# Performance work log

Measured on AMD Instinct MI355X. Metric: run time of the kernel, lower is better.

Reference implementation:

```python
import jax, jax.numpy as jnp
import numpy as np

B, LD, LQ = 32, 512, 32
E, NF = 300, 4
D = E + NF            # doc_input_size = 304
M = 16                # fofe_max_length == max_len
ALPHA = 0.9
VOCAB = 50000
H = 256
SAMPLE_NUM = 256
POS_N = 128           # int(sample_num * (1 - neg_ratio))
NEG_N = SAMPLE_NUM - POS_N
R = min(M, LD - 2)    # candidate negative lengths = 16
PPL = NEG_N // R + 1  # negatives drawn per length = 9


def setup_inputs() -> dict:
    key = jax.random.key(0)
    ks = jax.random.split(key, 16)
    emb = jax.random.normal(ks[0], (VOCAB, E), jnp.float32) * 0.1
    emb = emb.at[0].set(0.0)  # padding_idx=0
    doc = jax.random.randint(ks[1], (B, LD), 1, VOCAB)
    doc_f = jax.random.normal(ks[2], (B, LD, NF), jnp.float32) * 0.1
    query = jax.random.randint(ks[3], (B, LQ), 1, VOCAB)
    target_s = jax.random.randint(ks[4], (B,), 1, LD - M - 2)
    span = jax.random.randint(ks[5], (B,), 0, M)  # ans_span = target_e - target_s < fofe_max_length
    target_e = target_s + span
    rand_length = jax.random.permutation(ks[6], R)  # torch.randperm(min(max_len, L-2))
    # rand_position[i] ~ randint(1, LD - rand_length[i] - 1)
    u = jax.random.uniform(ks[7], (R, PPL))
    size = (LD - rand_length - 2).astype(jnp.float32)[:, None]
    rand_position = 1 + jnp.floor(u * size).astype(jnp.int32)
    rand_idx = jax.random.randint(ks[8], (NEG_N,), 0, B)  # faithful to original (dim-0 size used as bound)
    perm_idx = jax.random.permutation(ks[9], SAMPLE_NUM)

    def w(k, o, i):
        return jax.random.normal(k, (o, i), jnp.float32) * (1.0 / np.sqrt(i))

    CIN = 3 * D + E  # 1212
    W1 = w(ks[10], 4 * H, CIN)
    W2 = w(ks[11], 4 * H, 4 * H)
    W3 = w(ks[12], 4 * H, 4 * H)
    W4 = w(ks[13], 2 * H, 4 * H)
    W5 = w(ks[14], 1, 2 * H)
    doc_mask = jnp.zeros((B, LD), bool)
    query_mask = jnp.zeros((B, LQ), bool)
    return dict(doc=doc, doc_f=doc_f, query=query, target_s=target_s, target_e=target_e,
                doc_mask=doc_mask, query_mask=query_mask, emb=emb,
                W1=W1, W2=W2, W3=W3, W4=W4, W5=W5,
                rand_length=rand_length, rand_position=rand_position,
                rand_idx=rand_idx, perm_idx=perm_idx)


def _fofe_codes(x):
    """x: [B, D, LD] -> forward/inverse FOFE codes [B, D, M, LD].
    fwd[b,c,l,t] = sum_{k=0}^{l} alpha^k x[b,c,t-k]; inv mirrors to the right."""
    fwd_terms = jnp.stack(
        [(ALPHA ** k) * jnp.pad(x, ((0, 0), (0, 0), (k, 0)))[..., :LD] for k in range(M)], axis=2)
    inv_terms = jnp.stack(
        [(ALPHA ** k) * jnp.pad(x, ((0, 0), (0, 0), (0, k)))[..., k:] for k in range(M)], axis=2)
    return jnp.cumsum(fwd_terms, axis=2), jnp.cumsum(inv_terms, axis=2)


def _cnn(x, W1, W2, W3, W4, W5):
    h = jax.nn.relu(jnp.einsum('oi,bis->bos', W1, x))
    h = jax.nn.relu(jnp.einsum('oi,bis->bos', W2, h))
    h = jax.nn.relu(jnp.einsum('oi,bis->bos', W3, h))
    h = jax.nn.relu(jnp.einsum('oi,bis->bos', W4, h))
    return jax.nn.sigmoid(jnp.einsum('oi,bis->bos', W5, h))


def reference(doc, doc_f, query, target_s, target_e, doc_mask, query_mask, emb,
              W1, W2, W3, W4, W5, rand_length, rand_position, rand_idx, perm_idx):
    # input_embedding (dropout_emb = 0, pos/ner disabled)
    doc_input = jnp.concatenate([emb[doc], doc_f], axis=-1)  # [B, LD, D]
    x = jnp.swapaxes(doc_input, 1, 2)                         # [B, D, LD]
    fwd, inv = _fofe_codes(x)                                 # [B, D, M, LD] each

    # --- positive samples: gold span + left/right full contexts ---
    b = jnp.arange(B)
    span = target_e - target_s
    ans = fwd[b, :, span, target_e]                               # [B, D]
    l_ctx = fwd[b, :, M - 1, jnp.maximum(target_s - 1, 0)]        # [B, D]
    r_ctx = inv[b, :, M - 1, jnp.minimum(target_e + 1, LD - 1)]   # [B, D]
    pos = jnp.concatenate([l_ctx, ans, r_ctx], axis=-1)          # [B, 3D]
    pos = jnp.broadcast_to(pos[:, :, None], (B, 3 * D, POS_N))

    # --- negative samples: random spans of each length in rand_length ---
    rl = rand_length[:, None]                                     # [R, 1]
    neg_ans = fwd[:, :, rl, rand_position].reshape(B, D, R * PPL)
    neg_l = fwd[:, :, M - 1, rand_position - 1].reshape(B, D, R * PPL)
    neg_r = inv[:, :, M - 1, rand_position + rl + 1].reshape(B, D, R * PPL)
    rand_cat = jnp.concatenate([neg_l, neg_ans, neg_r], axis=1)   # [B, 3D, R*PPL]
    neg = rand_cat[:, :, rand_idx]                                # [B, 3D, NEG_N]

    # --- shuffle pos+neg, build query FOFE, run cnn, mse (sum) loss ---
    ctx_ans = jnp.concatenate([pos, neg], axis=-1)[:, :, perm_idx]
    target = jnp.concatenate(
        [jnp.ones((B, 1, POS_N), jnp.float32), jnp.zeros((B, 1, NEG_N), jnp.float32)],
        axis=-1)[:, :, perm_idx]
    qw = ALPHA ** jnp.arange(LQ - 1, -1, -1, dtype=jnp.float32)   # fofe_linear weights
    qf = jnp.einsum('t,bte->be', qw, emb[query])                  # [B, E]
    qb = jnp.broadcast_to(qf[:, :, None], (B, E, SAMPLE_NUM))
    dq_input = jnp.concatenate([ctx_ans, qb], axis=1)             # [B, 3D+E, S]
    score = _cnn(dq_input, W1, W2, W3, W4, W5)                    # [B, 1, S]
    loss = jnp.sum((score - target) ** 2)                         # mse_loss(size_average=False)
    return loss
```

## Files before the change

kernel.cpp:

```cpp
#include <hip/hip_runtime.h>
#include <hip/hip_bf16.h>

#define B_    32
#define LD_   512
#define LQ_   32
#define E_    300
#define NF_   4
#define D_    304
#define M_    16
#define ALPHA_ 0.9f
#define CIN_  1212
#define KP1_  1216
#define NCOL_ 1056
#define NPAD_ 1088
#define PPL_  9
#define NEG_N_ 128

typedef short short8 __attribute__((ext_vector_type(8)));
typedef float f32x4 __attribute__((ext_vector_type(4)));

__device__ __forceinline__ unsigned short f2bf(float f) {
    unsigned int x = __float_as_uint(f);
    unsigned int r = (x + 0x7FFFu + ((x >> 16) & 1u)) >> 16;
    return (unsigned short)r;
}
__device__ __forceinline__ float bf2f(unsigned short u) {
    return __uint_as_float(((unsigned int)u) << 16);
}

__global__ __launch_bounds__(256) void build_features(
    const int* __restrict__ doc, const float* __restrict__ doc_f,
    const int* __restrict__ query, const int* __restrict__ target_s,
    const int* __restrict__ target_e, const float* __restrict__ emb,
    const int* __restrict__ rand_length, const int* __restrict__ rand_position,
    unsigned short* __restrict__ Ft)
{
    int bcol = blockIdx.x;
    int b = bcol / 33;
    int col = bcol % 33;
    __shared__ int   s_t[3][16];
    __shared__ float s_w[3][16];
    __shared__ int   s_row[3][16];
    __shared__ int   s_qrow[32];
    __shared__ float s_qw[32];
    int tid = threadIdx.x;

    if (tid < 48) {
        int part = tid >> 4, k = tid & 15;
        int t; float valid;
        if (col == 0) {
            int ts = target_s[b], te = target_e[b];
            int span = te - ts;
            if (part == 0)      { t = ts - 1 - k;  valid = (t >= 0) ? 1.f : 0.f; }
            else if (part == 1) { t = te - k;      valid = (k <= span && t >= 0) ? 1.f : 0.f; }
            else                { t = te + 1 + k;  valid = (t < LD_) ? 1.f : 0.f; }
        } else {
            int j = col - 1;
            int r = j / PPL_, p = j - r * PPL_;
            int rl = rand_length[r];
            int rp = rand_position[r * PPL_ + p];
            if (part == 0)      { t = rp - 1 - k;      valid = (t >= 0) ? 1.f : 0.f; }
            else if (part == 1) { t = rp - k;          valid = (k <= rl && t >= 0) ? 1.f : 0.f; }
            else                { t = rp + rl + 1 + k; valid = (t < LD_) ? 1.f : 0.f; }
        }
        float w = (valid != 0.f) ? powf(ALPHA_, (float)k) : 0.f;
        t = min(max(t, 0), LD_ - 1);
        s_t[part][k] = t;
        s_w[part][k] = w;
        s_row[part][k] = doc[b * LD_ + t];
    }
    if (tid >= 64 && tid < 96) {
        int q = tid - 64;
        s_qrow[q] = query[b * LQ_ + q];
        s_qw[q] = powf(ALPHA_, (float)(LQ_ - 1 - q));
    }
    __syncthreads();

    unsigned short* out = Ft + (size_t)bcol * KP1_;
    for (int c = tid; c < KP1_; c += 256) {
        float acc = 0.f;
        if (c < 912) {
            int part = c / D_;
            int cc = c - part * D_;
            if (cc < E_) {
                for (int i = 0; i < 16; ++i)
                    acc += s_w[part][i] * emb[(size_t)s_row[part][i] * E_ + cc];
            } else {
                int f = cc - E_;
                for (int i = 0; i < 16; ++i)
                    acc += s_w[part][i] * doc_f[(b * LD_ + s_t[part][i]) * NF_ + f];
            }
        } else if (c < CIN_) {
            int ce = c - 912;
            for (int i = 0; i < 32; ++i)
                acc += s_qw[i] * emb[(size_t)s_qrow[i] * E_ + ce];
        }
        out[c] = f2bf(acc);
    }
}

__global__ __launch_bounds__(256) void convert_all(
    const float* __restrict__ W1, const float* __restrict__ W2,
    const float* __restrict__ W3, const float* __restrict__ W4,
    unsigned short* __restrict__ W1b, unsigned short* __restrict__ W2b,
    unsigned short* __restrict__ W3b, unsigned short* __restrict__ W4b)
{
    const long n1 = 1024L * KP1_;
    const long n2 = 1024L * 1024L;
    const long n4 = 512L * 1024L;
    const long total = n1 + 2 * n2 + n4;
    long stride = (long)gridDim.x * 256L;
    for (long i = (long)blockIdx.x * 256L + threadIdx.x; i < total; i += stride) {
        if (i < n1) {
            long m = i / KP1_; int k = (int)(i - m * KP1_);
            float v = (k < CIN_) ? W1[m * CIN_ + k] : 0.f;
            W1b[i] = f2bf(v);
        } else if (i < n1 + n2) {
            long j = i - n1; W2b[j] = f2bf(W2[j]);
        } else if (i < n1 + 2 * n2) {
            long j = i - n1 - n2; W3b[j] = f2bf(W3[j]);
        } else {
            long j = i - n1 - 2 * n2; W4b[j] = f2bf(W4[j]);
        }
    }
}

__global__ __launch_bounds__(256) void gemm_relu(
    const unsigned short* __restrict__ A,
    const unsigned short* __restrict__ Bm,
    unsigned short* __restrict__ C,
    int M, int K)
{
    __shared__ unsigned short As[64][40];
    __shared__ unsigned short Bs[64][40];
    int tid = threadIdx.x;
    int m0 = blockIdx.x * 64;
    int n0 = blockIdx.y * 64;
    int w = tid >> 6, lane = tid & 63;
    int wm = (w >> 1) * 32, wn = (w & 1) * 32;
    int lr = tid >> 2;
    int ls = (tid & 3) * 8;
    int fr = lane & 15;
    int fk = (lane >> 4) * 8;

    f32x4 acc00 = {0.f, 0.f, 0.f, 0.f};
    f32x4 acc01 = {0.f, 0.f, 0.f, 0.f};
    f32x4 acc10 = {0.f, 0.f, 0.f, 0.f};
    f32x4 acc11 = {0.f, 0.f, 0.f, 0.f};

    for (int k0 = 0; k0 < K; k0 += 32) {
        *(uint4*)(&As[lr][ls]) = *(const uint4*)(A + (size_t)(m0 + lr) * K + k0 + ls);
        *(uint4*)(&Bs[lr][ls]) = *(const uint4*)(Bm + (size_t)(n0 + lr) * K + k0 + ls);
        __syncthreads();
        short8 a0 = *(const short8*)(&As[wm + fr][fk]);
        short8 a1 = *(const short8*)(&As[wm + 16 + fr][fk]);
        short8 b0 = *(const short8*)(&Bs[wn + fr][fk]);
        short8 b1 = *(const short8*)(&Bs[wn + 16 + fr][fk]);
        acc00 = __builtin_amdgcn_mfma_f32_16x16x32_bf16(a0, b0, acc00, 0, 0, 0);
        acc01 = __builtin_amdgcn_mfma_f32_16x16x32_bf16(a0, b1, acc01, 0, 0, 0);
        acc10 = __builtin_amdgcn_mfma_f32_16x16x32_bf16(a1, b0, acc10, 0, 0, 0);
        acc11 = __builtin_amdgcn_mfma_f32_16x16x32_bf16(a1, b1, acc11, 0, 0, 0);
        __syncthreads();
    }

    int rbase = (lane >> 4) * 4;
    int cb = lane & 15;
    #define STORE_TILE(ACC, MT, NT) do {                                   \
        int m = m0 + wm + (MT) * 16 + rbase;                               \
        int n = n0 + wn + (NT) * 16 + cb;                                  \
        ushort4 o;                                                         \
        o.x = f2bf(fmaxf((ACC)[0], 0.f));                                  \
        o.y = f2bf(fmaxf((ACC)[1], 0.f));                                  \
        o.z = f2bf(fmaxf((ACC)[2], 0.f));                                  \
        o.w = f2bf(fmaxf((ACC)[3], 0.f));                                  \
        *(ushort4*)(C + (size_t)n * M + m) = o;                            \
    } while (0)
    STORE_TILE(acc00, 0, 0);
    STORE_TILE(acc01, 0, 1);
    STORE_TILE(acc10, 1, 0);
    STORE_TILE(acc11, 1, 1);
    #undef STORE_TILE
}

__global__ __launch_bounds__(256) void score_kernel(
    const unsigned short* __restrict__ h4,
    const float* __restrict__ W5, float* __restrict__ scores)
{
    int w = threadIdx.x >> 6, lane = threadIdx.x & 63;
    int col = blockIdx.x * 4 + w;
    if (col >= NCOL_) return;
    const unsigned short* row = h4 + (size_t)col * 512 + lane * 8;
    ushort4 v0 = *(const ushort4*)row;
    ushort4 v1 = *(const ushort4*)(row + 4);
    const float* w5 = W5 + lane * 8;
    float z = bf2f(v0.x) * w5[0] + bf2f(v0.y) * w5[1] +
              bf2f(v0.z) * w5[2] + bf2f(v0.w) * w5[3] +
              bf2f(v1.x) * w5[4] + bf2f(v1.y) * w5[5] +
              bf2f(v1.z) * w5[6] + bf2f(v1.w) * w5[7];
    for (int off = 32; off > 0; off >>= 1) z += __shfl_down(z, off, 64);
    if (lane == 0) scores[col] = 1.f / (1.f + expf(-z));
}

__global__ __launch_bounds__(256) void loss_kernel(
    const float* __restrict__ scores, const int* __restrict__ rand_idx,
    float* __restrict__ out)
{
    __shared__ int cnt[32];
    __shared__ float red[256];
    int tid = threadIdx.x;
    if (tid < 32) cnt[tid] = 0;
    __syncthreads();
    if (tid < NEG_N_) atomicAdd(&cnt[rand_idx[tid]], 1);
    __syncthreads();
    float acc = 0.f;
    for (int c = tid; c < NCOL_; c += 256) {
        int c33 = c % 33;
        float s = scores[c];
        if (c33 == 0) { float d = s - 1.f; acc += 128.f * d * d; }
        else          { acc += (float)cnt[c33 - 1] * s * s; }
    }
    red[tid] = acc;
    __syncthreads();
    for (int off = 128; off > 0; off >>= 1) {
        if (tid < off) red[tid] += red[tid + off];
        __syncthreads();
    }
    if (tid == 0) out[0] = red[0];
}

extern "C" void kernel_launch(void* const* d_in, const int* in_sizes, int n_in,
                              void* d_out, int out_size, void* d_ws, size_t ws_size,
                              hipStream_t stream)
{
    const int*   doc        = (const int*)d_in[0];
    const float* doc_f      = (const float*)d_in[1];
    const int*   query      = (const int*)d_in[2];
    const int*   target_s   = (const int*)d_in[3];
    const int*   target_e   = (const int*)d_in[4];
    const float* emb        = (const float*)d_in[7];
    const float* W1         = (const float*)d_in[8];
    const float* W2         = (const float*)d_in[9];
    const float* W3         = (const float*)d_in[10];
    const float* W4         = (const float*)d_in[11];
    const float* W5         = (const float*)d_in[12];
    const int*   rand_length   = (const int*)d_in[13];
    const int*   rand_position = (const int*)d_in[14];
    const int*   rand_idx      = (const int*)d_in[15];

    char* ws = (char*)d_ws;
    size_t off = 0;
    auto alloc = [&](size_t bytes) {
        void* p = ws + off;
        off = (off + bytes + 255) & ~(size_t)255;
        return p;
    };
    unsigned short* W1b = (unsigned short*)alloc((size_t)1024 * KP1_ * 2);
    unsigned short* W2b = (unsigned short*)alloc((size_t)1024 * 1024 * 2);
    unsigned short* W3b = (unsigned short*)alloc((size_t)1024 * 1024 * 2);
    unsigned short* W4b = (unsigned short*)alloc((size_t)512 * 1024 * 2);
    unsigned short* Ft  = (unsigned short*)alloc((size_t)NPAD_ * KP1_ * 2);
    unsigned short* hA  = (unsigned short*)alloc((size_t)NPAD_ * 1024 * 2);
    unsigned short* hB  = (unsigned short*)alloc((size_t)NPAD_ * 1024 * 2);
    float* scores       = (float*)alloc(NCOL_ * sizeof(float));
    (void)ws_size; (void)in_sizes; (void)n_in; (void)out_size;

    hipMemsetAsync(Ft + (size_t)NCOL_ * KP1_, 0,
                   (size_t)(NPAD_ - NCOL_) * KP1_ * 2, stream);

    convert_all<<<dim3(2048), dim3(256), 0, stream>>>(W1, W2, W3, W4,
                                                      W1b, W2b, W3b, W4b);
    build_features<<<dim3(NCOL_), dim3(256), 0, stream>>>(
        doc, doc_f, query, target_s, target_e, emb,
        rand_length, rand_position, Ft);

    gemm_relu<<<dim3(16, 17), dim3(256), 0, stream>>>(W1b, Ft, hA, 1024, KP1_);
    gemm_relu<<<dim3(16, 17), dim3(256), 0, stream>>>(W2b, hA, hB, 1024, 1024);
    gemm_relu<<<dim3(16, 17), dim3(256), 0, stream>>>(W3b, hB, hA, 1024, 1024);
    gemm_relu<<<dim3(8, 17),  dim3(256), 0, stream>>>(W4b, hA, hB, 512, 1024);

    score_kernel<<<dim3((NCOL_ + 3) / 4), dim3(256), 0, stream>>>(hB, W5, scores);
    loss_kernel<<<dim3(1), dim3(256), 0, stream>>>(scores, rand_idx, (float*)d_out);
}
```

Before: 231.8 us.

## Vectorize feature/weight kernels, double-buffer GEMM, hoist query FOFE, fuse score+loss

The query FOFE is now computed once per batch in its own kernel instead of in each of the 33 column blocks. build_features and the weight bf16 conversion now move data with float4 loads and ushort4 stores. The GEMM switches to a 64-wide K tile with double-buffered shared memory and register prefetch of the next tile, so there is one barrier per step. Score and loss are fused into one kernel that accumulates the loss with an atomic add, which adds a memset of the output and gives a nondeterministic summation order.

Result: faster. 195.1 us (-15.8%).

```diff
diff --git a/kernel.cpp b/kernel.cpp
--- a/kernel.cpp
+++ b/kernel.cpp
@@ -28,11 +28,40 @@
     return __uint_as_float(((unsigned int)u) << 16);
 }
 
-__global__ __launch_bounds__(256) void build_features(
+__global__ __launch_bounds__(128) void query_fofe(
+    const int* __restrict__ query, const float* __restrict__ emb,
+    unsigned short* __restrict__ qfb)
+{
+    int b = blockIdx.x;
+    __shared__ int   rows[32];
+    __shared__ float wq[32];
+    int tid = threadIdx.x;
+    if (tid < 32) {
+        rows[tid] = query[b * LQ_ + tid];
+        wq[tid] = powf(ALPHA_, (float)(LQ_ - 1 - tid));
+    }
+    __syncthreads();
+    if (tid < 76) {
+        int cc = tid * 4;
+        float ax = 0.f, ay = 0.f, az = 0.f, aw = 0.f;
+        if (cc < 300) {
+            for (int i = 0; i < 32; ++i) {
+                float4 v = *(const float4*)(emb + (size_t)rows[i] * E_ + cc);
+                float wv = wq[i];
+                ax += wv * v.x; ay += wv * v.y; az += wv * v.z; aw += wv * v.w;
+            }
+        }
+        ushort4 o; o.x = f2bf(ax); o.y = f2bf(ay); o.z = f2bf(az); o.w = f2bf(aw);
+        *(ushort4*)(qfb + (size_t)b * 304 + cc) = o;
+    }
+}
+
+__global__ __launch_bounds__(320) void build_features(
     const int* __restrict__ doc, const float* __restrict__ doc_f,
-    const int* __restrict__ query, const int* __restrict__ target_s,
-    const int* __restrict__ target_e, const float* __restrict__ emb,
+    const int* __restrict__ target_s, const int* __restrict__ target_e,
+    const float* __restrict__ emb,
     const int* __restrict__ rand_length, const int* __restrict__ rand_position,
+    const unsigned short* __restrict__ qfb,
     unsigned short* __restrict__ Ft)
 {
     int bcol = blockIdx.x;
@@ -41,8 +70,6 @@
     __shared__ int   s_t[3][16];
     __shared__ float s_w[3][16];
     __shared__ int   s_row[3][16];
-    __shared__ int   s_qrow[32];
-    __shared__ float s_qw[32];
     int tid = threadIdx.x;
 
     if (tid < 48) {
@@ -69,33 +96,36 @@
         s_w[part][k] = w;
         s_row[part][k] = doc[b * LD_ + t];
     }
-    if (tid >= 64 && tid < 96) {
-        int q = tid - 64;
-        s_qrow[q] = query[b * LQ_ + q];
-        s_qw[q] = powf(ALPHA_, (float)(LQ_ - 1 - q));
-    }
     __syncthreads();
 
     unsigned short* out = Ft + (size_t)bcol * KP1_;
-    for (int c = tid; c < KP1_; c += 256) {
-        float acc = 0.f;
-        if (c < 912) {
-            int part = c / D_;
-            int cc = c - part * D_;
-            if (cc < E_) {
-                for (int i = 0; i < 16; ++i)
-                    acc += s_w[part][i] * emb[(size_t)s_row[part][i] * E_ + cc];
-            } else {
-                int f = cc - E_;
-                for (int i = 0; i < 16; ++i)
-                    acc += s_w[part][i] * doc_f[(b * LD_ + s_t[part][i]) * NF_ + f];
+    int g = tid;
+    if (g < 228) {
+        int part = g / 76;
+        int g2 = g - part * 76;
+        int cc = g2 * 4;
+        float ax = 0.f, ay = 0.f, az = 0.f, aw = 0.f;
+        if (cc < 300) {
+            for (int i = 0; i < 16; ++i) {
+                float4 v = *(const float4*)(emb + (size_t)s_row[part][i] * E_ + cc);
+                float wv = s_w[part][i];
+                ax += wv * v.x; ay += wv * v.y; az += wv * v.z; aw += wv * v.w;
             }
-        } else if (c < CIN_) {
-            int ce = c - 912;
-            for (int i = 0; i < 32; ++i)
-                acc += s_qw[i] * emb[(size_t)s_qrow[i] * E_ + ce];
-        }
-        out[c] = f2bf(acc);
+        } else {
+            for (int i = 0; i < 16; ++i) {
+                float4 v = *(const float4*)(doc_f + ((size_t)b * LD_ + s_t[part][i]) * NF_);
+                float wv = s_w[part][i];
+                ax += wv * v.x; ay += wv * v.y; az += wv * v.z; aw += wv * v.w;
+            }
+        }
+        ushort4 o; o.x = f2bf(ax); o.y = f2bf(ay); o.z = f2bf(az); o.w = f2bf(aw);
+        *(ushort4*)(out + 4 * g) = o;
+    } else if (g < 303) {
+        *(ushort4*)(out + 4 * g) =
+            *(const ushort4*)(qfb + (size_t)b * 304 + (g - 228) * 4);
+    } else if (g == 303) {
+        ushort4 z; z.x = 0; z.y = 0; z.z = 0; z.w = 0;
+        *(ushort4*)(out + 4 * g) = z;
     }
 }
 
@@ -105,22 +135,35 @@
     unsigned short* __restrict__ W1b, unsigned short* __restrict__ W2b,
     unsigned short* __restrict__ W3b, unsigned short* __restrict__ W4b)
 {
-    const long n1 = 1024L * KP1_;
-    const long n2 = 1024L * 1024L;
-    const long n4 = 512L * 1024L;
+    const long n1 = 1024L * KP1_ / 4;
+    const long n2 = 1024L * 1024L / 4;
+    const long n4 = 512L * 1024L / 4;
     const long total = n1 + 2 * n2 + n4;
     long stride = (long)gridDim.x * 256L;
     for (long i = (long)blockIdx.x * 256L + threadIdx.x; i < total; i += stride) {
+        ushort4 o;
         if (i < n1) {
-            long m = i / KP1_; int k = (int)(i - m * KP1_);
-            float v = (k < CIN_) ? W1[m * CIN_ + k] : 0.f;
-            W1b[i] = f2bf(v);
+            long m = i / 304; int k4 = (int)(i - m * 304);
+            if (k4 < 303) {
+                float4 v = *(const float4*)(W1 + m * CIN_ + k4 * 4);
+                o.x = f2bf(v.x); o.y = f2bf(v.y); o.z = f2bf(v.z); o.w = f2bf(v.w);
+            } else { o.x = 0; o.y = 0; o.z = 0; o.w = 0; }
+            *(ushort4*)(W1b + i * 4) = o;
         } else if (i < n1 + n2) {
-            long j = i - n1; W2b[j] = f2bf(W2[j]);
+            long j = i - n1;
+            float4 v = *(const float4*)(W2 + j * 4);
+            o.x = f2bf(v.x); o.y = f2bf(v.y); o.z = f2bf(v.z); o.w = f2bf(v.w);
+            *(ushort4*)(W2b + j * 4) = o;
         } else if (i < n1 + 2 * n2) {
-            long j = i - n1 - n2; W3b[j] = f2bf(W3[j]);
+            long j = i - n1 - n2;
+            float4 v = *(const float4*)(W3 + j * 4);
+            o.x = f2bf(v.x); o.y = f2bf(v.y); o.z = f2bf(v.z); o.w = f2bf(v.w);
+            *(ushort4*)(W3b + j * 4) = o;
         } else {
-            long j = i - n1 - 2 * n2; W4b[j] = f2bf(W4[j]);
+            long j = i - n1 - 2 * n2;
+            float4 v = *(const float4*)(W4 + j * 4);
+            o.x = f2bf(v.x); o.y = f2bf(v.y); o.z = f2bf(v.z); o.w = f2bf(v.w);
+            *(ushort4*)(W4b + j * 4) = o;
         }
     }
 }
@@ -131,36 +174,66 @@
     unsigned short* __restrict__ C,
     int M, int K)
 {
-    __shared__ unsigned short As[64][40];
-    __shared__ unsigned short Bs[64][40];
+    __shared__ unsigned short As[2][64][72];
+    __shared__ unsigned short Bs[2][64][72];
     int tid = threadIdx.x;
-    int m0 = blockIdx.x * 64;
-    int n0 = blockIdx.y * 64;
+    int m0 = blockIdx.x * 64, n0 = blockIdx.y * 64;
     int w = tid >> 6, lane = tid & 63;
     int wm = (w >> 1) * 32, wn = (w & 1) * 32;
     int lr = tid >> 2;
-    int ls = (tid & 3) * 8;
-    int fr = lane & 15;
-    int fk = (lane >> 4) * 8;
-
-    f32x4 acc00 = {0.f, 0.f, 0.f, 0.f};
-    f32x4 acc01 = {0.f, 0.f, 0.f, 0.f};
-    f32x4 acc10 = {0.f, 0.f, 0.f, 0.f};
-    f32x4 acc11 = {0.f, 0.f, 0.f, 0.f};
-
-    for (int k0 = 0; k0 < K; k0 += 32) {
-        *(uint4*)(&As[lr][ls]) = *(const uint4*)(A + (size_t)(m0 + lr) * K + k0 + ls);
-        *(uint4*)(&Bs[lr][ls]) = *(const uint4*)(Bm + (size_t)(n0 + lr) * K + k0 + ls);
+    int ls = (tid & 3) * 16;
+    int fr = lane & 15, fk = (lane >> 4) * 8;
+
+    const unsigned short* Arow = A + (size_t)(m0 + lr) * K + ls;
+    const unsigned short* Brow = Bm + (size_t)(n0 + lr) * K + ls;
+
+    f32x4 acc00 = {0.f,0.f,0.f,0.f}, acc01 = {0.f,0.f,0.f,0.f};
+    f32x4 acc10 = {0.f,0.f,0.f,0.f}, acc11 = {0.f,0.f,0.f,0.f};
+
+    int nk = K >> 6;
+    {
+        uint4 a0 = *(const uint4*)(Arow);
+        uint4 a1 = *(const uint4*)(Arow + 8);
+        uint4 b0 = *(const uint4*)(Brow);
+        uint4 b1 = *(const uint4*)(Brow + 8);
+        *(uint4*)&As[0][lr][ls]     = a0;
+        *(uint4*)&As[0][lr][ls + 8] = a1;
+        *(uint4*)&Bs[0][lr][ls]     = b0;
+        *(uint4*)&Bs[0][lr][ls + 8] = b1;
+    }
+    __syncthreads();
+    int cur = 0;
+    for (int i = 0; i < nk; ++i) {
+        uint4 na0, na1, nb0, nb1;
+        bool more = (i + 1 < nk);
+        if (more) {
+            const unsigned short* An = Arow + (size_t)(i + 1) * 64;
+            const unsigned short* Bn = Brow + (size_t)(i + 1) * 64;
+            na0 = *(const uint4*)(An);
+            na1 = *(const uint4*)(An + 8);
+            nb0 = *(const uint4*)(Bn);
+            nb1 = *(const uint4*)(Bn + 8);
+        }
+        #pragma unroll
+        for (int s = 0; s < 2; ++s) {
+            short8 fa0 = *(const short8*)&As[cur][wm + fr][s * 32 + fk];
+            short8 fa1 = *(const short8*)&As[cur][wm + 16 + fr][s * 32 + fk];
+            short8 fb0 = *(const short8*)&Bs[cur][wn + fr][s * 32 + fk];
+            short8 fb1 = *(const short8*)&Bs[cur][wn + 16 + fr][s * 32 + fk];
+            acc00 = __builtin_amdgcn_mfma_f32_16x16x32_bf16(fa0, fb0, acc00, 0, 0, 0);
+            acc01 = __builtin_amdgcn_mfma_f32_16x16x32_bf16(fa0, fb1, acc01, 0, 0, 0);
+            acc10 = __builtin_amdgcn_mfma_f32_16x16x32_bf16(fa1, fb0, acc10, 0, 0, 0);
+            acc11 = __builtin_amdgcn_mfma_f32_16x16x32_bf16(fa1, fb1, acc11, 0, 0, 0);
+        }
+        if (more) {
+            int nb = cur ^ 1;
+            *(uint4*)&As[nb][lr][ls]     = na0;
+            *(uint4*)&As[nb][lr][ls + 8] = na1;
+            *(uint4*)&Bs[nb][lr][ls]     = nb0;
+            *(uint4*)&Bs[nb][lr][ls + 8] = nb1;
+        }
         __syncthreads();
-        short8 a0 = *(const short8*)(&As[wm + fr][fk]);
-        short8 a1 = *(const short8*)(&As[wm + 16 + fr][fk]);
-        short8 b0 = *(const short8*)(&Bs[wn + fr][fk]);
-        short8 b1 = *(const short8*)(&Bs[wn + 16 + fr][fk]);
-        acc00 = __builtin_amdgcn_mfma_f32_16x16x32_bf16(a0, b0, acc00, 0, 0, 0);
-        acc01 = __builtin_amdgcn_mfma_f32_16x16x32_bf16(a0, b1, acc01, 0, 0, 0);
-        acc10 = __builtin_amdgcn_mfma_f32_16x16x32_bf16(a1, b0, acc10, 0, 0, 0);
-        acc11 = __builtin_amdgcn_mfma_f32_16x16x32_bf16(a1, b1, acc11, 0, 0, 0);
-        __syncthreads();
+        cur ^= 1;
     }
 
     int rbase = (lane >> 4) * 4;
@@ -182,13 +255,21 @@
     #undef STORE_TILE
 }
 
-__global__ __launch_bounds__(256) void score_kernel(
+__global__ __launch_bounds__(256) void score_loss(
     const unsigned short* __restrict__ h4,
-    const float* __restrict__ W5, float* __restrict__ scores)
-{
-    int w = threadIdx.x >> 6, lane = threadIdx.x & 63;
+    const float* __restrict__ W5, const int* __restrict__ rand_idx,
+    float* __restrict__ out)
+{
+    __shared__ int cnt[32];
+    __shared__ float part[4];
+    int tid = threadIdx.x;
+    if (tid < 32) cnt[tid] = 0;
+    __syncthreads();
+    if (tid < NEG_N_) atomicAdd(&cnt[rand_idx[tid]], 1);
+    __syncthreads();
+    int w = tid >> 6, lane = tid & 63;
     int col = blockIdx.x * 4 + w;
-    if (col >= NCOL_) return;
+    float v = 0.f;
     const unsigned short* row = h4 + (size_t)col * 512 + lane * 8;
     ushort4 v0 = *(const ushort4*)row;
     ushort4 v1 = *(const ushort4*)(row + 4);
@@ -198,34 +279,15 @@
               bf2f(v1.x) * w5[4] + bf2f(v1.y) * w5[5] +
               bf2f(v1.z) * w5[6] + bf2f(v1.w) * w5[7];
     for (int off = 32; off > 0; off >>= 1) z += __shfl_down(z, off, 64);
-    if (lane == 0) scores[col] = 1.f / (1.f + expf(-z));
-}
-
-__global__ __launch_bounds__(256) void loss_kernel(
-    const float* __restrict__ scores, const int* __restrict__ rand_idx,
-    float* __restrict__ out)
-{
-    __shared__ int cnt[32];
-    __shared__ float red[256];
-    int tid = threadIdx.x;
-    if (tid < 32) cnt[tid] = 0;
-    __syncthreads();
-    if (tid < NEG_N_) atomicAdd(&cnt[rand_idx[tid]], 1);
-    __syncthreads();
-    float acc = 0.f;
-    for (int c = tid; c < NCOL_; c += 256) {
-        int c33 = c % 33;
-        float s = scores[c];
-        if (c33 == 0) { float d = s - 1.f; acc += 128.f * d * d; }
-        else          { acc += (float)cnt[c33 - 1] * s * s; }
-    }
-    red[tid] = acc;
-    __syncthreads();
-    for (int off = 128; off > 0; off >>= 1) {
-        if (tid < off) red[tid] += red[tid + off];
-        __syncthreads();
-    }
-    if (tid == 0) out[0] = red[0];
+    if (lane == 0) {
+        float s = 1.f / (1.f + expf(-z));
+        int c33 = col % 33;
+        if (c33 == 0) { float d = s - 1.f; v = 128.f * d * d; }
+        else          { v = (float)cnt[c33 - 1] * s * s; }
+        part[w] = v;
+    }
+    __syncthreads();
+    if (tid == 0) atomicAdd(out, part[0] + part[1] + part[2] + part[3]);
 }
 
 extern "C" void kernel_launch(void* const* d_in, const int* in_sizes, int n_in,
@@ -261,23 +323,25 @@
     unsigned short* Ft  = (unsigned short*)alloc((size_t)NPAD_ * KP1_ * 2);
     unsigned short* hA  = (unsigned short*)alloc((size_t)NPAD_ * 1024 * 2);
     unsigned short* hB  = (unsigned short*)alloc((size_t)NPAD_ * 1024 * 2);
-    float* scores       = (float*)alloc(NCOL_ * sizeof(float));
+    unsigned short* qfb = (unsigned short*)alloc((size_t)B_ * 304 * 2);
+    float* d_loss = (float*)d_out;
     (void)ws_size; (void)in_sizes; (void)n_in; (void)out_size;
 
     hipMemsetAsync(Ft + (size_t)NCOL_ * KP1_, 0,
                    (size_t)(NPAD_ - NCOL_) * KP1_ * 2, stream);
-
-    convert_all<<<dim3(2048), dim3(256), 0, stream>>>(W1, W2, W3, W4,
+    hipMemsetAsync(d_loss, 0, sizeof(float), stream);
+
+    convert_all<<<dim3(3776), dim3(256), 0, stream>>>(W1, W2, W3, W4,
                                                       W1b, W2b, W3b, W4b);
-    build_features<<<dim3(NCOL_), dim3(256), 0, stream>>>(
-        doc, doc_f, query, target_s, target_e, emb,
-        rand_length, rand_position, Ft);
+    query_fofe<<<dim3(B_), dim3(128), 0, stream>>>(query, emb, qfb);
+    build_features<<<dim3(NCOL_), dim3(320), 0, stream>>>(
+        doc, doc_f, target_s, target_e, emb,
+        rand_length, rand_position, qfb, Ft);
 
     gemm_relu<<<dim3(16, 17), dim3(256), 0, stream>>>(W1b, Ft, hA, 1024, KP1_);
     gemm_relu<<<dim3(16, 17), dim3(256), 0, stream>>>(W2b, hA, hB, 1024, 1024);
     gemm_relu<<<dim3(16, 17), dim3(256), 0, stream>>>(W3b, hB, hA, 1024, 1024);
     gemm_relu<<<dim3(8, 17),  dim3(256), 0, stream>>>(W4b, hA, hB, 512, 1024);
 
-    score_kernel<<<dim3((NCOL_ + 3) / 4), dim3(256), 0, stream>>>(hB, W5, scores);
-    loss_kernel<<<dim3(1), dim3(256), 0, stream>>>(scores, rand_idx, (float*)d_out);
-}
+    score_loss<<<dim3(NCOL_ / 4), dim3(256), 0, stream>>>(hB, W5, rand_idx, d_loss);
+}
```
